# Kernel tuning notes

Hardware: AMD Instinct MI355X
Metric: run time of the kernel (lower is better)

The kernel has to match this reference:

```python
import jax, jax.numpy as jnp
import numpy as np

B, C, L, HEADS, DK = 32, 128, 32, 8, 64  # batch, channels, lattice side (L1=L2=L), heads, head dim
NLAYER = 4


def setup_inputs() -> dict:
    key = jax.random.key(0)
    ks = jax.random.split(key, 6)
    s_in = 1.0 / float(np.sqrt(C))          # lecun-normal scale for QKV (fan_in = channels)
    s_out = 1.0 / float(np.sqrt(HEADS * DK))  # lecun-normal scale for W0 (fan_in = dk*heads)
    return {
        "x": jax.random.normal(ks[0], (B, C, L, L), jnp.float32),
        "Wq": jax.random.normal(ks[1], (HEADS * DK, C), jnp.float32) * s_in,
        "Wk": jax.random.normal(ks[2], (HEADS * DK, C), jnp.float32) * s_in,
        "Wv": jax.random.normal(ks[3], (HEADS * DK, C), jnp.float32) * s_in,
        "R": jax.random.normal(ks[4], (HEADS, L, L), jnp.float32) * 0.02,
        "W0": jax.random.normal(ks[5], (C, HEADS * DK), jnp.float32) * s_out,
    }


def get_irpe(R):
    # r[h, i, j] = R[h, (xi - xj) mod L1, (yi - yj) mod L2]  (jnp negative indexing wraps)
    heads, L1, L2 = R.shape
    a1 = jnp.arange(L1)
    a2 = jnp.arange(L2)
    dx = (a1[:, None] - a1[None, :]) % L1        # (L1, L1)
    dy = (a2[:, None] - a2[None, :]) % L2        # (L2, L2)
    bias = R[:, dx[:, None, :, None], dy[None, :, None, :]]  # (heads, L1, L2, L1, L2)
    return bias.reshape(heads, L1 * L2, L1 * L2)


def reference(x, Wq, Wk, Wv, R, W0):
    bias = get_irpe(R)                            # (heads, N, N)
    inv_layer = 1.0 / float(np.sqrt(NLAYER + 1))
    inv_sqrt_dk = 1.0 / float(np.sqrt(DK))

    def block(xs):  # xs: (C, L, L) — single sample, as in the original __call__
        xn = xs * inv_layer
        xf = xn.reshape(C, -1)                    # (C, N)
        Q = (Wq @ xf).reshape(HEADS, DK, -1)      # 1x1 conv == matmul
        K = (Wk @ xf).reshape(HEADS, DK, -1)
        V = (Wv @ xf).reshape(HEADS, DK, -1)
        dot = jnp.einsum('hdi,hdj->hij', Q, K) + bias
        alpha = jax.nn.softmax(dot * inv_sqrt_dk, axis=-1)
        att = jnp.einsum('hij,hdj->hdi', alpha, V).reshape(HEADS * DK, -1)
        return (W0 @ att).reshape(xs.shape) + xs  # residual

    return jax.vmap(block)(x)
```

## Files before the change

kernel.cpp:

```cpp
#include <hip/hip_runtime.h>


#define NB   32
#define NH   8
#define SEQ  1024
#define DKH  64
#define HDIM 512
#define CIN  128

#define SCL 0.18033688011112042f

typedef __bf16 bf16x8 __attribute__((ext_vector_type(8)));
typedef float floatx4 __attribute__((ext_vector_type(4)));
typedef unsigned short u16x8 __attribute__((ext_vector_type(8)));
typedef unsigned int uintx4 __attribute__((ext_vector_type(4)));

__device__ __forceinline__ unsigned short f2bf(float f) {
    union { float f; unsigned int u; } c; c.f = f;
    unsigned int u = c.u;
    return (unsigned short)((u + 0x7fffu + ((u >> 16) & 1u)) >> 16);
}
__device__ __forceinline__ bf16x8 ldfrag(const unsigned short* p) {
    u16x8 v = *reinterpret_cast<const u16x8*>(p);
    return __builtin_bit_cast(bf16x8, v);
}
__device__ __forceinline__ unsigned int pkbf(float a, float b) {
    unsigned int ua = __builtin_bit_cast(unsigned int, a);
    unsigned int ub = __builtin_bit_cast(unsigned int, b);
    ua += 0x7fffu + ((ua >> 16) & 1u);
    ub += 0x7fffu + ((ub >> 16) & 1u);
    return __builtin_amdgcn_perm(ub, ua, 0x07060302u);
}
__device__ __forceinline__ unsigned int pkbf_t(float a, float b) {
    return __builtin_amdgcn_perm(__builtin_bit_cast(unsigned int, b),
                                 __builtin_bit_cast(unsigned int, a), 0x07060302u);
}
__device__ __forceinline__ void g2l16(const void* g, void* l) {
    __builtin_amdgcn_global_load_lds((const __attribute__((address_space(1))) void*)g,
                                     (__attribute__((address_space(3))) void*)l, 16, 0, 0);
}


__global__ __launch_bounds__(256) void prep_all(const float* __restrict__ Wq,
                                                const float* __restrict__ Wk,
                                                const float* __restrict__ Wv,
                                                const float* __restrict__ W0,
                                                const float* __restrict__ R,
                                                const float* __restrict__ x,
                                                unsigned short* __restrict__ w2,
                                                unsigned short* __restrict__ w0f,
                                                float* __restrict__ biasQ4,
                                                unsigned short* __restrict__ xt2) {
    __shared__ float lds[64 * 65];
    int bid = blockIdx.x;
    if (bid < 32) {
        int idx4 = bid * 256 + threadIdx.x;
        int st = idx4 & 31, dxx = (idx4 >> 5) & 31, h = idx4 >> 10;
        const float* Rh = R + (h << 10) + (dxx << 5);
        floatx4 v;
        for (int r = 0; r < 4; ++r) v[r] = Rh[(32 - st - r) & 31] * SCL;
        *(floatx4*)&biasQ4[(size_t)idx4 * 4] = v;
    } else if (bid < 1056) {
        int idx = (bid - 32) * 256 + threadIdx.x;
        if (idx < 196608) {
            int row = idx >> 7, col = idx & 127;
            float v;
            if (row < 512)       v = Wq[idx] * SCL;
            else if (row < 1024) v = Wk[idx - 65536];
            else                 v = Wv[idx - 131072];
            int rt = row >> 4, nr = row & 15, kc = col >> 5, qc = (col & 31) >> 3, jc = col & 7;
            w2[((rt * 4 + kc) * 512) + (qc * 16 + nr) * 8 + jc] = f2bf(v);
        } else {
            int idx2 = idx - 196608;
            int row = idx2 >> 9, col = idx2 & 511;
            int rt = row >> 4, nr = row & 15, kcA = col >> 5, qc = (col & 31) >> 3, jc = col & 7;
            w0f[((rt * 16 + kcA) * 512) + (qc * 16 + nr) * 8 + jc] = f2bf(W0[idx2]);
        }
    } else {
        int r = bid - 1056;
        int b = r & 31, yy = (r >> 5) & 1, zz = r >> 6;
        int c0 = yy * 64, p0 = zz * 64;
        int t = threadIdx.x, tr = t >> 6, tc = t & 63;
        const float inv_layer = 0.44721359549995793f;
        for (int rr = 0; rr < 16; ++rr) {
            int cl = rr * 4 + tr;
            lds[cl * 65 + tc] = x[(b * CIN + c0 + cl) * SEQ + p0 + tc];
        }
        __syncthreads();
        for (int rr = 0; rr < 16; ++rr) {
            int pl = rr * 4 + tr;
            int pos = p0 + pl, c = c0 + tc;
            int pt = pos >> 4, np = pos & 15, kc = c >> 5, qc = (c & 31) >> 3, jc = c & 7;
            xt2[((size_t)((b * 64 + pt) * 4 + kc) * 512) + (qc * 16 + np) * 8 + jc] =
                f2bf(lds[tc * 65 + pl] * inv_layer);
        }
    }
}

__global__ __launch_bounds__(256, 2) void qkv_gemm(const unsigned short* __restrict__ xt2,
                                                   const unsigned short* __restrict__ w2,
                                                   unsigned short* __restrict__ Qt,
                                                   unsigned short* __restrict__ Kf,
                                                   unsigned short* __restrict__ Vf) {
    int b = blockIdx.x, y = blockIdx.y, zt = blockIdx.z;
    int tid = threadIdx.x, wave = tid >> 6, lane = tid & 63, q = lane >> 4, n = lane & 15;
    floatx4 acc[4];
    for (int s = 0; s < 4; ++s) acc[s] = (floatx4){0.f, 0.f, 0.f, 0.f};
    bf16x8 af[4], bfr[4][4];
    if (y < 16) {
        int rt = y * 4 + wave;
        const unsigned short* wbase = w2 + (size_t)rt * 4 * 512 + lane * 8;
        const unsigned short* xbase = xt2 + (size_t)(b * 64 + zt * 4) * 4 * 512 + lane * 8;
        for (int kc = 0; kc < 4; ++kc) af[kc] = ldfrag(wbase + kc * 512);
        for (int s = 0; s < 4; ++s)
            for (int kc = 0; kc < 4; ++kc) bfr[s][kc] = ldfrag(xbase + (s * 4 + kc) * 512);
        for (int kc = 0; kc < 4; ++kc)
            for (int s = 0; s < 4; ++s)
                acc[s] = __builtin_amdgcn_mfma_f32_16x16x32_bf16(af[kc], bfr[s][kc], acc[s], 0, 0, 0);
        int wrow0 = y * 64 + wave * 16;
        int pos0 = zt * 64;
        if (y < 8) {
            int h = wrow0 >> 6;
            int d0 = (wrow0 & 63) + 4 * q;
            for (int s = 0; s < 4; ++s) {
                uint2 pk;
                pk.x = pkbf(acc[s][0], acc[s][1]);
                pk.y = pkbf(acc[s][2], acc[s][3]);
                int pos = pos0 + 16 * s + n;
                *(uint2*)&Qt[((size_t)(b * NH + h) * SEQ + pos) * DKH + d0] = pk;
            }
        } else {
            int h = (wrow0 >> 6) - 8;
            int bh = b * NH + h;
            int cd = wave >> 1;
            int qk = 2 * (wave & 1) + (q >> 1);
            int jk = 4 * (q & 1);
            for (int s = 0; s < 4; ++s) {
                uint2 pk;
                pk.x = pkbf(acc[s][0], acc[s][1]);
                pk.y = pkbf(acc[s][2], acc[s][3]);
                size_t addr = ((size_t)(bh * 16 + zt) * 8 + s * 2 + cd) * 512
                              + (qk * 16 + n) * 8 + jk;
                *(uint2*)&Kf[addr] = pk;
            }
        }
    } else {
        int pt = zt * 4 + wave;
        const unsigned short* xbase = xt2 + (size_t)((b * 64 + pt) * 4) * 512 + lane * 8;
        int rtv0 = 64 + (y - 16) * 4;
        const unsigned short* wbase = w2 + (size_t)rtv0 * 4 * 512 + lane * 8;
        for (int kc = 0; kc < 4; ++kc) af[kc] = ldfrag(xbase + kc * 512);
        for (int s = 0; s < 4; ++s)
            for (int kc = 0; kc < 4; ++kc) bfr[s][kc] = ldfrag(wbase + (s * 4 + kc) * 512);
        for (int kc = 0; kc < 4; ++kc)
            for (int s = 0; s < 4; ++s)
                acc[s] = __builtin_amdgcn_mfma_f32_16x16x32_bf16(af[kc], bfr[s][kc], acc[s], 0, 0, 0);
        int vrow0 = (y - 16) * 64;
        int cj = wave >> 1;
        int jj0 = 4 * (wave & 1);
        for (int s = 0; s < 4; ++s) {
            int vrow = vrow0 + 16 * s + n;
            int h = vrow >> 6, d = vrow & 63;
            int u = d >> 4, nl = d & 15;
            uint2 pk;
            pk.x = pkbf(acc[s][0], acc[s][1]);
            pk.y = pkbf(acc[s][2], acc[s][3]);
            size_t addr = ((size_t)((b * NH + h) * 16 + zt) * 8 + u * 2 + cj) * 512
                          + (q * 16 + nl) * 8 + jj0;
            *(uint2*)&Vf[addr] = pk;
        }
    }
}

__global__ __launch_bounds__(256, 2) void attn_kernel(const unsigned short* __restrict__ Qt,
                                                      const unsigned short* __restrict__ Kf,
                                                      const unsigned short* __restrict__ Vf,
                                                      const float* __restrict__ biasQ4,
                                                      unsigned short* __restrict__ att2) {
    __shared__ alignas(16) unsigned short lds_k[2][8 * 512];
    __shared__ alignas(16) unsigned short lds_v[2][8 * 512];
    __shared__ alignas(16) float lds_bQ[4096];

    int gid = blockIdx.x;
    int bh = gid & 255, qb = gid >> 8;
    int b = bh >> 3, h = bh & 7;
    int tid = threadIdx.x, wave = tid >> 6, lane = tid & 63, q = lane >> 4, n = lane & 15;
    int i0 = qb * 256 + wave * 64;
    int ti0 = i0 >> 4;

    const unsigned short* qbase = Qt + (size_t)bh * SEQ * DKH;
    const unsigned short* kft = Kf + (size_t)bh * 16 * 4096;
    const unsigned short* vft = Vf + (size_t)bh * 16 * 4096;
    int off0 = wave * 512;

    {
        const float* bQg = biasQ4 + (size_t)h * 4096;
        for (int i = 0; i < 4; ++i) {
            int fo = i * 1024 + wave * 256;
            g2l16(bQg + fo + lane * 4, &lds_bQ[fo]);
        }
        g2l16(kft + off0 + lane * 8,        &lds_k[0][off0]);
        g2l16(kft + 2048 + off0 + lane * 8, &lds_k[0][2048 + off0]);
        g2l16(vft + off0 + lane * 8,        &lds_v[0][off0]);
        g2l16(vft + 2048 + off0 + lane * 8, &lds_v[0][2048 + off0]);
    }

    bf16x8 aq[4][2];
    for (int qt = 0; qt < 4; ++qt)
        for (int c = 0; c < 2; ++c)
            aq[qt][c] = ldfrag(qbase + (i0 + 16 * qt + n) * DKH + c * 32 + q * 8);

    floatx4 o[4][4];
    float lsum[4] = {0.f, 0.f, 0.f, 0.f};
    for (int qt = 0; qt < 4; ++qt)
        for (int u = 0; u < 4; ++u) o[qt][u] = (floatx4){0.f, 0.f, 0.f, 0.f};

    int st0_4 = ((4 * q - n) & 31) * 4;
    int st1_4 = (((4 * q - n) + 16) & 31) * 4;
    int ee64 = qb * 8 + 2 * wave + 256;

    __syncthreads();

#define LDB(qt, s0, s1, s2, s3) do {                                          \
        int eh_ = ee64 + ((qt) >> 1);                                         \
        int dh_ = (eh_ & 31) << 7;                                            \
        int dl_ = ((eh_ - 1) & 31) << 7;                                      \
        int sa_ = ((qt) & 1) ? st1_4 : st0_4;                                 \
        int sb_ = ((qt) & 1) ? st0_4 : st1_4;                                 \
        s0 = *(const floatx4*)&lds_bQ[dh_ + sa_];                             \
        s1 = *(const floatx4*)&lds_bQ[dh_ + sb_];                             \
        s2 = *(const floatx4*)&lds_bQ[dl_ + sa_];                             \
        s3 = *(const floatx4*)&lds_bQ[dl_ + sb_];                             \
    } while (0)

#define SMM(qt, s0, s1, s2, s3) do {                                          \
        s0 = __builtin_amdgcn_mfma_f32_16x16x32_bf16(kf2[0][0], aq[qt][0], s0, 0, 0, 0); \
        s0 = __builtin_amdgcn_mfma_f32_16x16x32_bf16(kf2[0][1], aq[qt][1], s0, 0, 0, 0); \
        s1 = __builtin_amdgcn_mfma_f32_16x16x32_bf16(kf2[1][0], aq[qt][0], s1, 0, 0, 0); \
        s1 = __builtin_amdgcn_mfma_f32_16x16x32_bf16(kf2[1][1], aq[qt][1], s1, 0, 0, 0); \
        s2 = __builtin_amdgcn_mfma_f32_16x16x32_bf16(kf2[2][0], aq[qt][0], s2, 0, 0, 0); \
        s2 = __builtin_amdgcn_mfma_f32_16x16x32_bf16(kf2[2][1], aq[qt][1], s2, 0, 0, 0); \
        s3 = __builtin_amdgcn_mfma_f32_16x16x32_bf16(kf2[3][0], aq[qt][0], s3, 0, 0, 0); \
        s3 = __builtin_amdgcn_mfma_f32_16x16x32_bf16(kf2[3][1], aq[qt][1], s3, 0, 0, 0); \
    } while (0)

#define EPO(qt, s0, s1, s2, s3) do {                                          \
        floatx4 e0_, e1_, e2_, e3_;                                           \
        for (int r_ = 0; r_ < 4; ++r_) {                                      \
            e0_[r_] = __builtin_amdgcn_exp2f(s0[r_]);                         \
            e1_[r_] = __builtin_amdgcn_exp2f(s1[r_]);                         \
            e2_[r_] = __builtin_amdgcn_exp2f(s2[r_]);                         \
            e3_[r_] = __builtin_amdgcn_exp2f(s3[r_]);                         \
        }                                                                     \
        uintx4 pu0_, pu1_;                                                    \
        pu0_[0] = pkbf_t(e0_[0], e0_[1]);                                     \
        pu0_[1] = pkbf_t(e0_[2], e0_[3]);                                     \
        pu0_[2] = pkbf_t(e1_[0], e1_[1]);                                     \
        pu0_[3] = pkbf_t(e1_[2], e1_[3]);                                     \
        pu1_[0] = pkbf_t(e2_[0], e2_[1]);                                     \
        pu1_[1] = pkbf_t(e2_[2], e2_[3]);                                     \
        pu1_[2] = pkbf_t(e3_[0], e3_[1]);                                     \
        pu1_[3] = pkbf_t(e3_[2], e3_[3]);                                     \
        bf16x8 pf0_ = __builtin_bit_cast(bf16x8, pu0_);                       \
        bf16x8 pf1_ = __builtin_bit_cast(bf16x8, pu1_);                       \
        floatx4 es_ = (e0_ + e1_) + (e2_ + e3_);                              \
        lsum[qt] += (es_[0] + es_[1]) + (es_[2] + es_[3]);                    \
        o[qt][0] = __builtin_amdgcn_mfma_f32_16x16x32_bf16(vf2[0][0], pf0_, o[qt][0], 0, 0, 0); \
        o[qt][0] = __builtin_amdgcn_mfma_f32_16x16x32_bf16(vf2[0][1], pf1_, o[qt][0], 0, 0, 0); \
        o[qt][1] = __builtin_amdgcn_mfma_f32_16x16x32_bf16(vf2[1][0], pf0_, o[qt][1], 0, 0, 0); \
        o[qt][1] = __builtin_amdgcn_mfma_f32_16x16x32_bf16(vf2[1][1], pf1_, o[qt][1], 0, 0, 0); \
        o[qt][2] = __builtin_amdgcn_mfma_f32_16x16x32_bf16(vf2[2][0], pf0_, o[qt][2], 0, 0, 0); \
        o[qt][2] = __builtin_amdgcn_mfma_f32_16x16x32_bf16(vf2[2][1], pf1_, o[qt][2], 0, 0, 0); \
        o[qt][3] = __builtin_amdgcn_mfma_f32_16x16x32_bf16(vf2[3][0], pf0_, o[qt][3], 0, 0, 0); \
        o[qt][3] = __builtin_amdgcn_mfma_f32_16x16x32_bf16(vf2[3][1], pf1_, o[qt][3], 0, 0, 0); \
    } while (0)

    for (int kt = 0; kt < 16; ++kt) {
        int cur = kt & 1;

        if (kt < 15) {
            const unsigned short* kg = kft + (kt + 1) * 4096;
            const unsigned short* vg = vft + (kt + 1) * 4096;
            unsigned short* dk = &lds_k[cur ^ 1][0];
            unsigned short* dv = &lds_v[cur ^ 1][0];
            g2l16(kg + off0 + lane * 8,        dk + off0);
            g2l16(kg + 2048 + off0 + lane * 8, dk + 2048 + off0);
            g2l16(vg + off0 + lane * 8,        dv + off0);
            g2l16(vg + 2048 + off0 + lane * 8, dv + 2048 + off0);
        }

        bf16x8 kf2[4][2], vf2[4][2];
#pragma unroll
        for (int s = 0; s < 4; ++s)
#pragma unroll
            for (int c = 0; c < 2; ++c) {
                kf2[s][c] = ldfrag(&lds_k[cur][(s * 2 + c) * 512 + lane * 8]);
                vf2[s][c] = ldfrag(&lds_v[cur][(s * 2 + c) * 512 + lane * 8]);
            }

        floatx4 s0, s1, s2, s3;
        LDB(0, s0, s1, s2, s3);
        SMM(0, s0, s1, s2, s3);
        EPO(0, s0, s1, s2, s3);
        LDB(1, s0, s1, s2, s3);
        SMM(1, s0, s1, s2, s3);
        EPO(1, s0, s1, s2, s3);
        LDB(2, s0, s1, s2, s3);
        SMM(2, s0, s1, s2, s3);
        EPO(2, s0, s1, s2, s3);
        LDB(3, s0, s1, s2, s3);
        SMM(3, s0, s1, s2, s3);
        EPO(3, s0, s1, s2, s3);

        ee64 -= 2;
        __syncthreads();
    }

#undef LDB
#undef SMM
#undef EPO

    for (int qt = 0; qt < 4; ++qt) {
        float ls = lsum[qt];
        ls += __shfl_xor(ls, 16, 64);
        ls += __shfl_xor(ls, 32, 64);
        float inv = 1.0f / ls;
        int pt = ti0 + qt;
        for (int u = 0; u < 4; ++u) {
            int kcA = 2 * h + (u >> 1);
            int q2 = 2 * (u & 1) + (q >> 1);
            uint2 pk;
            pk.x = pkbf(o[qt][u][0] * inv, o[qt][u][1] * inv);
            pk.y = pkbf(o[qt][u][2] * inv, o[qt][u][3] * inv);
            size_t addr = ((size_t)((b * 64 + pt) * 16 + kcA) * 512)
                          + (q2 * 16 + n) * 8 + 4 * (q & 1);
            *(uint2*)&att2[addr] = pk;
        }
    }
}

__global__ __launch_bounds__(256, 2) void out_gemm(const unsigned short* __restrict__ att2,
                                                   const unsigned short* __restrict__ w0f,
                                                   const float* __restrict__ x,
                                                   float* __restrict__ out) {
    int b = blockIdx.x, ct = blockIdx.y, ptb = blockIdx.z;
    int tid = threadIdx.x, wave = tid >> 6, lane = tid & 63, q = lane >> 4, n = lane & 15;
    int pos0 = ptb * 64 + wave * 16;
    int c0 = ct * 64;
    int pt = ptb * 4 + wave;
    const unsigned short* abase = att2 + (size_t)(b * 64 + pt) * 16 * 512 + lane * 8;
    const unsigned short* wbase = w0f + (size_t)(c0 >> 4) * 16 * 512 + lane * 8;
    floatx4 acc[4];
    for (int s = 0; s < 4; ++s) acc[s] = (floatx4){0.f, 0.f, 0.f, 0.f};
    for (int g = 0; g < 4; ++g) {
        bf16x8 af[4], bfr[4][4];
        for (int k2 = 0; k2 < 4; ++k2) af[k2] = ldfrag(abase + (g * 4 + k2) * 512);
        for (int s = 0; s < 4; ++s)
            for (int k2 = 0; k2 < 4; ++k2)
                bfr[s][k2] = ldfrag(wbase + (s * 16 + g * 4 + k2) * 512);
        for (int k2 = 0; k2 < 4; ++k2)
            for (int s = 0; s < 4; ++s)
                acc[s] = __builtin_amdgcn_mfma_f32_16x16x32_bf16(af[k2], bfr[s][k2], acc[s], 0, 0, 0);
    }
    int p0q = pos0 + 4 * q;
    for (int s = 0; s < 4; ++s) {
        int c = c0 + 16 * s + n;
        size_t idx = ((size_t)b * CIN + c) * SEQ + p0q;
        floatx4 res = *(const floatx4*)&x[idx];
        floatx4 v = acc[s] + res;
        *(floatx4*)&out[idx] = v;
    }
}

extern "C" void kernel_launch(void* const* d_in, const int* in_sizes, int n_in,
                              void* d_out, int out_size, void* d_ws, size_t ws_size,
                              hipStream_t stream) {
    const float* x  = (const float*)d_in[0];
    const float* Wq = (const float*)d_in[1];
    const float* Wk = (const float*)d_in[2];
    const float* Wv = (const float*)d_in[3];
    const float* R  = (const float*)d_in[4];
    const float* W0 = (const float*)d_in[5];
    float* out = (float*)d_out;

    char* ws = (char*)d_ws;
    size_t off = 0;
    unsigned short* Qt   = (unsigned short*)(ws + off); off += (size_t)NB * NH * SEQ * DKH * 2;
    unsigned short* Kf   = (unsigned short*)(ws + off); off += (size_t)NB * NH * SEQ * DKH * 2;
    unsigned short* Vf   = (unsigned short*)(ws + off); off += (size_t)NB * NH * SEQ * DKH * 2;
    unsigned short* att2 = (unsigned short*)(ws + off); off += (size_t)NB * SEQ * HDIM * 2;
    unsigned short* xt2  = (unsigned short*)(ws + off); off += (size_t)NB * SEQ * CIN * 2;
    unsigned short* w2   = (unsigned short*)(ws + off); off += (size_t)1536 * 128 * 2;
    unsigned short* w0f  = (unsigned short*)(ws + off); off += (size_t)128 * 512 * 2;
    float* biasQ4 = (float*)(ws + off); off += (size_t)NH * 32 * 32 * 4 * 4;
    (void)ws_size; (void)in_sizes; (void)n_in; (void)out_size;

    prep_all<<<2080, 256, 0, stream>>>(Wq, Wk, Wv, W0, R, x, w2, w0f, biasQ4, xt2);
    qkv_gemm<<<dim3(NB, 24, 16), 256, 0, stream>>>(xt2, w2, Qt, Kf, Vf);
    attn_kernel<<<NB * NH * 4, 256, 0, stream>>>(Qt, Kf, Vf, biasQ4, att2);
    out_gemm<<<dim3(NB, 2, 16), 256, 0, stream>>>(att2, w0f, x, out);
}
```

Before: 209.5 us.

## Stage shared GEMM operand through LDS in qkv and output projection kernels

In qkv_gemm, the operand that all four waves read identically (the x tile for Q/K, the weight tile for V) is now loaded once into LDS with async global-to-LDS copies. Each wave then reads its fragments from LDS instead of issuing redundant global loads. out_gemm similarly stages W0 fragments in a double-buffered LDS area, prefetching the next K-chunk while computing the current one. Launch bounds are raised to 3 blocks per CU to cut register pressure, at the cost of added barriers and LDS usage.

New measurement: 192.0 us. 1.09x faster.

```diff
diff --git a/kernel.cpp b/kernel.cpp
--- a/kernel.cpp
+++ b/kernel.cpp
@@ -97,26 +97,39 @@
     }
 }
 
-__global__ __launch_bounds__(256, 2) void qkv_gemm(const unsigned short* __restrict__ xt2,
+__global__ __launch_bounds__(256, 3) void qkv_gemm(const unsigned short* __restrict__ xt2,
                                                    const unsigned short* __restrict__ w2,
                                                    unsigned short* __restrict__ Qt,
                                                    unsigned short* __restrict__ Kf,
                                                    unsigned short* __restrict__ Vf) {
+    __shared__ alignas(16) unsigned short lds_s[16 * 512];
     int b = blockIdx.x, y = blockIdx.y, zt = blockIdx.z;
     int tid = threadIdx.x, wave = tid >> 6, lane = tid & 63, q = lane >> 4, n = lane & 15;
     floatx4 acc[4];
     for (int s = 0; s < 4; ++s) acc[s] = (floatx4){0.f, 0.f, 0.f, 0.f};
-    bf16x8 af[4], bfr[4][4];
+    bf16x8 af[4];
+
     if (y < 16) {
+        const unsigned short* xsrc = xt2 + (size_t)(b * 64 + zt * 4) * 4 * 512;
+        for (int i = 0; i < 4; ++i) {
+            int f = wave * 4 + i;
+            g2l16(xsrc + f * 512 + lane * 8, &lds_s[f * 512]);
+        }
         int rt = y * 4 + wave;
         const unsigned short* wbase = w2 + (size_t)rt * 4 * 512 + lane * 8;
-        const unsigned short* xbase = xt2 + (size_t)(b * 64 + zt * 4) * 4 * 512 + lane * 8;
         for (int kc = 0; kc < 4; ++kc) af[kc] = ldfrag(wbase + kc * 512);
-        for (int s = 0; s < 4; ++s)
-            for (int kc = 0; kc < 4; ++kc) bfr[s][kc] = ldfrag(xbase + (s * 4 + kc) * 512);
-        for (int kc = 0; kc < 4; ++kc)
-            for (int s = 0; s < 4; ++s)
-                acc[s] = __builtin_amdgcn_mfma_f32_16x16x32_bf16(af[kc], bfr[s][kc], acc[s], 0, 0, 0);
+        __syncthreads();
+#pragma unroll
+        for (int kc = 0; kc < 4; ++kc) {
+            bf16x8 b0 = ldfrag(&lds_s[(0 * 4 + kc) * 512 + lane * 8]);
+            bf16x8 b1 = ldfrag(&lds_s[(1 * 4 + kc) * 512 + lane * 8]);
+            bf16x8 b2 = ldfrag(&lds_s[(2 * 4 + kc) * 512 + lane * 8]);
+            bf16x8 b3 = ldfrag(&lds_s[(3 * 4 + kc) * 512 + lane * 8]);
+            acc[0] = __builtin_amdgcn_mfma_f32_16x16x32_bf16(af[kc], b0, acc[0], 0, 0, 0);
+            acc[1] = __builtin_amdgcn_mfma_f32_16x16x32_bf16(af[kc], b1, acc[1], 0, 0, 0);
+            acc[2] = __builtin_amdgcn_mfma_f32_16x16x32_bf16(af[kc], b2, acc[2], 0, 0, 0);
+            acc[3] = __builtin_amdgcn_mfma_f32_16x16x32_bf16(af[kc], b3, acc[3], 0, 0, 0);
+        }
         int wrow0 = y * 64 + wave * 16;
         int pos0 = zt * 64;
         if (y < 8) {
@@ -145,16 +158,26 @@
             }
         }
     } else {
+        const unsigned short* wsrc = w2 + (size_t)(64 + (y - 16) * 4) * 4 * 512;
+        for (int i = 0; i < 4; ++i) {
+            int f = wave * 4 + i;
+            g2l16(wsrc + f * 512 + lane * 8, &lds_s[f * 512]);
+        }
         int pt = zt * 4 + wave;
-        const unsigned short* xbase = xt2 + (size_t)((b * 64 + pt) * 4) * 512 + lane * 8;
-        int rtv0 = 64 + (y - 16) * 4;
-        const unsigned short* wbase = w2 + (size_t)rtv0 * 4 * 512 + lane * 8;
+        const unsigned short* xbase = xt2 + (size_t)(b * 64 + pt) * 4 * 512 + lane * 8;
         for (int kc = 0; kc < 4; ++kc) af[kc] = ldfrag(xbase + kc * 512);
-        for (int s = 0; s < 4; ++s)
-            for (int kc = 0; kc < 4; ++kc) bfr[s][kc] = ldfrag(wbase + (s * 4 + kc) * 512);
-        for (int kc = 0; kc < 4; ++kc)
-            for (int s = 0; s < 4; ++s)
-                acc[s] = __builtin_amdgcn_mfma_f32_16x16x32_bf16(af[kc], bfr[s][kc], acc[s], 0, 0, 0);
+        __syncthreads();
+#pragma unroll
+        for (int kc = 0; kc < 4; ++kc) {
+            bf16x8 b0 = ldfrag(&lds_s[(0 * 4 + kc) * 512 + lane * 8]);
+            bf16x8 b1 = ldfrag(&lds_s[(1 * 4 + kc) * 512 + lane * 8]);
+            bf16x8 b2 = ldfrag(&lds_s[(2 * 4 + kc) * 512 + lane * 8]);
+            bf16x8 b3 = ldfrag(&lds_s[(3 * 4 + kc) * 512 + lane * 8]);
+            acc[0] = __builtin_amdgcn_mfma_f32_16x16x32_bf16(af[kc], b0, acc[0], 0, 0, 0);
+            acc[1] = __builtin_amdgcn_mfma_f32_16x16x32_bf16(af[kc], b1, acc[1], 0, 0, 0);
+            acc[2] = __builtin_amdgcn_mfma_f32_16x16x32_bf16(af[kc], b2, acc[2], 0, 0, 0);
+            acc[3] = __builtin_amdgcn_mfma_f32_16x16x32_bf16(af[kc], b3, acc[3], 0, 0, 0);
+        }
         int vrow0 = (y - 16) * 64;
         int cj = wave >> 1;
         int jj0 = 4 * (wave & 1);
@@ -339,29 +362,48 @@
     }
 }
 
-__global__ __launch_bounds__(256, 2) void out_gemm(const unsigned short* __restrict__ att2,
+__global__ __launch_bounds__(256, 3) void out_gemm(const unsigned short* __restrict__ att2,
                                                    const unsigned short* __restrict__ w0f,
                                                    const float* __restrict__ x,
                                                    float* __restrict__ out) {
+    __shared__ alignas(16) unsigned short lds_w[2][16 * 512];
     int b = blockIdx.x, ct = blockIdx.y, ptb = blockIdx.z;
     int tid = threadIdx.x, wave = tid >> 6, lane = tid & 63, q = lane >> 4, n = lane & 15;
     int pos0 = ptb * 64 + wave * 16;
     int c0 = ct * 64;
     int pt = ptb * 4 + wave;
     const unsigned short* abase = att2 + (size_t)(b * 64 + pt) * 16 * 512 + lane * 8;
-    const unsigned short* wbase = w0f + (size_t)(c0 >> 4) * 16 * 512 + lane * 8;
+    const unsigned short* wsrc = w0f + (size_t)(c0 >> 4) * 16 * 512;
     floatx4 acc[4];
     for (int s = 0; s < 4; ++s) acc[s] = (floatx4){0.f, 0.f, 0.f, 0.f};
+
+    for (int k2 = 0; k2 < 4; ++k2)
+        g2l16(wsrc + (wave * 16 + k2) * 512 + lane * 8, &lds_w[0][(wave * 4 + k2) * 512]);
+    __syncthreads();
+
     for (int g = 0; g < 4; ++g) {
-        bf16x8 af[4], bfr[4][4];
+        int buf = g & 1;
+        if (g < 3) {
+            for (int k2 = 0; k2 < 4; ++k2)
+                g2l16(wsrc + (wave * 16 + (g + 1) * 4 + k2) * 512 + lane * 8,
+                      &lds_w[buf ^ 1][(wave * 4 + k2) * 512]);
+        }
+        bf16x8 af[4];
         for (int k2 = 0; k2 < 4; ++k2) af[k2] = ldfrag(abase + (g * 4 + k2) * 512);
-        for (int s = 0; s < 4; ++s)
-            for (int k2 = 0; k2 < 4; ++k2)
-                bfr[s][k2] = ldfrag(wbase + (s * 16 + g * 4 + k2) * 512);
-        for (int k2 = 0; k2 < 4; ++k2)
-            for (int s = 0; s < 4; ++s)
-                acc[s] = __builtin_amdgcn_mfma_f32_16x16x32_bf16(af[k2], bfr[s][k2], acc[s], 0, 0, 0);
-    }
+#pragma unroll
+        for (int k2 = 0; k2 < 4; ++k2) {
+            bf16x8 b0 = ldfrag(&lds_w[buf][(0 * 4 + k2) * 512 + lane * 8]);
+            bf16x8 b1 = ldfrag(&lds_w[buf][(1 * 4 + k2) * 512 + lane * 8]);
+            bf16x8 b2 = ldfrag(&lds_w[buf][(2 * 4 + k2) * 512 + lane * 8]);
+            bf16x8 b3 = ldfrag(&lds_w[buf][(3 * 4 + k2) * 512 + lane * 8]);
+            acc[0] = __builtin_amdgcn_mfma_f32_16x16x32_bf16(af[k2], b0, acc[0], 0, 0, 0);
+            acc[1] = __builtin_amdgcn_mfma_f32_16x16x32_bf16(af[k2], b1, acc[1], 0, 0, 0);
+            acc[2] = __builtin_amdgcn_mfma_f32_16x16x32_bf16(af[k2], b2, acc[2], 0, 0, 0);
+            acc[3] = __builtin_amdgcn_mfma_f32_16x16x32_bf16(af[k2], b3, acc[3], 0, 0, 0);
+        }
+        __syncthreads();
+    }
+
     int p0q = pos0 + 4 * q;
     for (int s = 0; s < 4; ++s) {
         int c = c0 + 16 * s + n;
```
